# Performance work log

Measured on AMD Instinct MI355X. Metric: run time of the kernel, lower is better.

## Reference

```python
import jax, jax.numpy as jnp
import numpy as np

D_MODEL, D_STATE, D_CONV, D_INNER, DT_RANK, K = 96, 16, 3, 192, 6, 4
B, H, W = 1, 64, 64


def setup_inputs() -> dict:
    key = jax.random.key(0)
    ks = jax.random.split(key, 10)
    x = jax.random.normal(ks[0], (B, H, W, D_MODEL), jnp.float32)
    in_proj_w = jax.random.normal(ks[1], (2 * D_INNER, D_MODEL), jnp.float32) * 0.02
    conv_w = jax.random.normal(ks[2], (D_INNER, 1, D_CONV, D_CONV), jnp.float32) * 0.1
    conv_b = jnp.zeros((D_INNER,), jnp.float32)
    x_proj_w = jax.random.normal(ks[3], (K, DT_RANK + 2 * D_STATE, D_INNER), jnp.float32) * 0.02
    dt_std = DT_RANK ** -0.5
    dt_w = jax.random.uniform(ks[4], (K, D_INNER, DT_RANK), jnp.float32, -dt_std, dt_std)
    # dt bias init: inv-softplus of dt ~ logUniform(1e-3, 1e-1)
    u = jax.random.uniform(ks[5], (K, D_INNER), jnp.float32)
    dt = jnp.exp(u * (np.log(0.1) - np.log(0.001)) + np.log(0.001)).clip(1e-4)
    dt_b = dt + jnp.log(-jnp.expm1(-dt))
    A_logs = jnp.log(jnp.broadcast_to(jnp.arange(1, D_STATE + 1, dtype=jnp.float32), (K * D_INNER, D_STATE)))
    Ds = jnp.ones((K * D_INNER,), jnp.float32)
    ln_g = jnp.ones((D_INNER,), jnp.float32)
    ln_b = jnp.zeros((D_INNER,), jnp.float32)
    out_proj_w = jax.random.normal(ks[6], (D_MODEL, D_INNER), jnp.float32) * 0.02
    return dict(x=x, in_proj_w=in_proj_w, conv_w=conv_w, conv_b=conv_b, x_proj_w=x_proj_w,
                dt_w=dt_w, dt_b=dt_b, A_logs=A_logs, Ds=Ds, ln_g=ln_g, ln_b=ln_b,
                out_proj_w=out_proj_w)


def _ss2d(x, in_proj_w, conv_w, conv_b, x_proj_w, dt_w, dt_b, A_logs, Ds, ln_g, ln_b, out_proj_w):
    b, h, w, c = x.shape
    L = h * w
    d = conv_w.shape[0]            # d_inner
    n = A_logs.shape[1]            # d_state
    r = dt_w.shape[2]              # dt_rank
    # in_proj + split
    xz = jnp.einsum('bhwc,ec->bhwe', x, in_proj_w)
    xx, z = xz[..., :d], xz[..., d:]
    # depthwise conv (NCHW) + SiLU
    xc = xx.transpose(0, 3, 1, 2)
    pad = (D_CONV - 1) // 2
    xc = jax.lax.conv_general_dilated(xc, conv_w, (1, 1), [(pad, pad), (pad, pad)],
                                      feature_group_count=d) + conv_b[None, :, None, None]
    xc = jax.nn.silu(xc)
    # 4 scan directions: HW, WH, and their reverses
    x_hw = xc.reshape(b, d, L)
    x_wh = xc.transpose(0, 1, 3, 2).reshape(b, d, L)
    xs = jnp.stack([x_hw, x_wh, x_hw[..., ::-1], x_wh[..., ::-1]], axis=1)  # (b,K,d,L)
    x_dbl = jnp.einsum('bkdl,kcd->bkcl', xs, x_proj_w)
    dts, Bs, Cs = x_dbl[:, :, :r], x_dbl[:, :, r:r + n], x_dbl[:, :, r + n:]
    dts = jnp.einsum('bkrl,kdr->bkdl', dts, dt_w)
    delta = jax.nn.softplus(dts + dt_b[None, :, :, None])        # (b,K,d,L)
    A = -jnp.exp(A_logs).reshape(K, d, n)
    # time-major scanned inputs
    dA = jnp.exp(jnp.einsum('bkdl,kdn->lbkdn', delta, A))        # (L,b,K,d,n)
    dBu = jnp.einsum('bkdl,bknl,bkdl->lbkdn', delta, Bs, xs)
    Ct = Cs.transpose(3, 0, 1, 2)                                # (L,b,K,n)
    def step(hst, inp):
        dA_t, dBu_t, C_t = inp
        hst = dA_t * hst + dBu_t
        return hst, jnp.einsum('bkdn,bkn->bkd', hst, C_t)
    h0 = jnp.zeros((b, K, d, n), jnp.float32)
    _, ys = jax.lax.scan(step, h0, (dA, dBu, Ct))                # ys: (L,b,K,d)
    out_y = ys.transpose(1, 2, 3, 0) + xs * Ds.reshape(K, d)[None, :, :, None]
    # recombine directions
    inv = out_y[:, 2:4][..., ::-1]
    y1 = out_y[:, 0]
    y2 = inv[:, 0]
    wh = out_y[:, 1].reshape(b, d, w, h).transpose(0, 1, 3, 2).reshape(b, d, L)
    invwh = inv[:, 1].reshape(b, d, w, h).transpose(0, 1, 3, 2).reshape(b, d, L)
    y = (y1 + y2 + wh + invwh).transpose(0, 2, 1).reshape(b, h, w, d)
    # LayerNorm (eps=1e-5, torch default)
    mu = y.mean(-1, keepdims=True)
    var = ((y - mu) ** 2).mean(-1, keepdims=True)
    y = (y - mu) * jax.lax.rsqrt(var + 1e-5) * ln_g + ln_b
    y = y * jax.nn.silu(z)
    return jnp.einsum('bhwd,cd->bhwc', y, out_proj_w)


def reference(x, in_proj_w, conv_w, conv_b, x_proj_w, dt_w, dt_b, A_logs, Ds, ln_g, ln_b, out_proj_w):
    return _ss2d(x, in_proj_w, conv_w, conv_b, x_proj_w, dt_w, dt_b, A_logs, Ds, ln_g, ln_b, out_proj_w)
```

## Files before the change

### kernel.cpp

```cpp
#include <hip/hip_runtime.h>
#include <hip/hip_bf16.h>

#define LL 4096
#define DM 96
#define DI 192
#define NS 16
#define RK 6
#define RKP 8
#define KD 4
#define CPROJ 38
#define NCH (KD*DI)
#define NC (KD*DI*NS)
#define PT 32
#define WS 196
#define OT 8
#define L2E 1.44269504f

__device__ __forceinline__ float bf2f(unsigned short u){
  unsigned int x = ((unsigned int)u) << 16;
  return __uint_as_float(x);
}
__device__ __forceinline__ float b2f(__hip_bfloat16 v){ return __bfloat162float(v); }

__device__ __forceinline__ void detect_bf16(const unsigned short* __restrict__ xh, int tid, int* sflag){
  if (tid < 64){
    unsigned short u = xh[2*tid];
    int e = (u >> 7) & 0xFF;
    int sane = (e >= 107 && e <= 131) ? 1 : 0;
    unsigned long long m = __ballot(sane);
    if (tid == 0) *sflag = (__popcll(m) >= 32) ? 1 : 0;
  }
}

__device__ __forceinline__ int dir_map(int k, int t){
  if (k==0) return t;
  if (k==1) return ((t&63)<<6) | (t>>6);
  if (k==2) return 4095 - t;
  int u = 4095 - t; return ((u&63)<<6) | (u>>6);
}

struct P12 { const void* p[12]; };

__global__ void __launch_bounds__(384) k_inprojcvt(P12 ptrs, float* __restrict__ cvt,
                         float* __restrict__ xx, float* __restrict__ z) {
  __shared__ float xr[8*DM];
  __shared__ int sflag;
  int tid = threadIdx.x;
  detect_bf16((const unsigned short*)ptrs.p[0], tid, &sflag);
  __syncthreads();
  int f = sflag;
  if (blockIdx.x >= LL/8){
    const int off[12] = {0,36864,38592,38784,67968,72576,73344,85632,86400,86592,86784,105216};
    int i = (blockIdx.x - LL/8)*384 + tid + 36864;
    if (i < 105216){
      int j = 1;
      #pragma unroll
      for (int s = 2; s < 11; s++) if (i >= off[s]) j = s;
      int e = i - off[j];
      const void* src = ptrs.p[j+1];
      cvt[i] = f ? b2f(((const __hip_bfloat16*)src)[e]) : ((const float*)src)[e];
    }
    return;
  }
  int l0 = blockIdx.x * 8;
  if (f){
    const __hip_bfloat16* xb = (const __hip_bfloat16*)ptrs.p[0] + (size_t)l0*DM;
    for (int i = tid; i < 8*DM; i += 384) xr[i] = b2f(xb[i]);
  } else {
    const float* xf = (const float*)ptrs.p[0] + (size_t)l0*DM;
    for (int i = tid; i < 8*DM; i += 384) xr[i] = xf[i];
  }
  __syncthreads();
  int e = tid;
  float acc[8];
  #pragma unroll
  for (int i=0;i<8;i++) acc[i]=0.f;
  const float4* xr4 = (const float4*)xr;
  if (f){
    const ushort4* wb = (const ushort4*)((const unsigned short*)ptrs.p[1] + (size_t)e*DM);
    #pragma unroll 4
    for (int c4=0;c4<DM/4;c4++){
      ushort4 uv = wb[c4];
      float4 wv = make_float4(bf2f(uv.x), bf2f(uv.y), bf2f(uv.z), bf2f(uv.w));
      #pragma unroll
      for (int i=0;i<8;i++){
        float4 xv = xr4[i*24 + c4];
        acc[i] = fmaf(wv.x,xv.x,fmaf(wv.y,xv.y,fmaf(wv.z,xv.z,fmaf(wv.w,xv.w,acc[i]))));
      }
    }
  } else {
    const float4* wr4 = (const float4*)((const float*)ptrs.p[1] + (size_t)e*DM);
    #pragma unroll 4
    for (int c4=0;c4<DM/4;c4++){
      float4 wv = wr4[c4];
      #pragma unroll
      for (int i=0;i<8;i++){
        float4 xv = xr4[i*24 + c4];
        acc[i] = fmaf(wv.x,xv.x,fmaf(wv.y,xv.y,fmaf(wv.z,xv.z,fmaf(wv.w,xv.w,acc[i]))));
      }
    }
  }
  if (e < DI) {
    #pragma unroll
    for (int i=0;i<8;i++) xx[(l0+i)*DI + e] = acc[i];
  } else {
    int e2 = e - DI;
    #pragma unroll
    for (int i=0;i<8;i++) z[(l0+i)*DI + e2] = acc[i];
  }
}

__global__ void k_conv(const float* __restrict__ xx,
                       const float* __restrict__ cw,
                       const float* __restrict__ cb,
                       float* __restrict__ xc) {
  int l = blockIdx.x;
  int d = threadIdx.x;
  int h = l >> 6, w = l & 63;
  float acc = cb[d];
  #pragma unroll
  for (int ki=0; ki<3; ki++){
    int hh = h + ki - 1;
    if ((unsigned)hh >= 64u) continue;
    #pragma unroll
    for (int kj=0;kj<3;kj++){
      int wj = w + kj - 1;
      if ((unsigned)wj >= 64u) continue;
      acc = fmaf(cw[d*9 + ki*3 + kj], xx[(hh*64+wj)*DI + d], acc);
    }
  }
  float v = acc / (1.f + __expf(-acc));
  xc[l*DI + d] = v;
}

__global__ void __launch_bounds__(256) k_proj(const float* __restrict__ xc,
                       const float* __restrict__ xpw,
                       float* __restrict__ dts,
                       float* __restrict__ Bb, float* __restrict__ Cb) {
  __shared__ float wl[CPROJ*WS];
  __shared__ float xs[PT*WS];
  int b = blockIdx.x;
  int k = b >> 7;
  int t_base = (b & 127) * PT;
  int tid = threadIdx.x;
  for (int idx = tid; idx < CPROJ*DI; idx += 256){
    int cc = idx / DI, j = idx - cc*DI;
    wl[cc*WS + j] = xpw[(k*CPROJ + cc)*DI + j];
  }
  for (int idx = tid; idx < PT*DI; idx += 256){
    int tt = idx / DI, j = idx - tt*DI;
    xs[tt*WS + j] = xc[dir_map(k, t_base + tt)*DI + j];
  }
  __syncthreads();
  int tg = tid & 7;
  int ty = tid >> 3;
  int cc0 = ty;
  int has2 = (ty + 32 < CPROJ);
  int cc1 = has2 ? (ty + 32) : ty;
  float a0x=0.f,a0y=0.f,a0z=0.f,a0w=0.f;
  float a1x=0.f,a1y=0.f,a1z=0.f,a1w=0.f;
  const float4* w0p = (const float4*)&wl[cc0*WS];
  const float4* w1p = (const float4*)&wl[cc1*WS];
  const float4* x0p = (const float4*)&xs[(tg     )*WS];
  const float4* x1p = (const float4*)&xs[(tg +  8)*WS];
  const float4* x2p = (const float4*)&xs[(tg + 16)*WS];
  const float4* x3p = (const float4*)&xs[(tg + 24)*WS];
  #pragma unroll 4
  for (int jc = 0; jc < DI/4; jc++){
    float4 w0 = w0p[jc], w1 = w1p[jc];
    float4 x0 = x0p[jc], x1 = x1p[jc], x2 = x2p[jc], x3 = x3p[jc];
    a0x = fmaf(w0.x,x0.x,fmaf(w0.y,x0.y,fmaf(w0.z,x0.z,fmaf(w0.w,x0.w,a0x))));
    a0y = fmaf(w0.x,x1.x,fmaf(w0.y,x1.y,fmaf(w0.z,x1.z,fmaf(w0.w,x1.w,a0y))));
    a0z = fmaf(w0.x,x2.x,fmaf(w0.y,x2.y,fmaf(w0.z,x2.z,fmaf(w0.w,x2.w,a0z))));
    a0w = fmaf(w0.x,x3.x,fmaf(w0.y,x3.y,fmaf(w0.z,x3.z,fmaf(w0.w,x3.w,a0w))));
    a1x = fmaf(w1.x,x0.x,fmaf(w1.y,x0.y,fmaf(w1.z,x0.z,fmaf(w1.w,x0.w,a1x))));
    a1y = fmaf(w1.x,x1.x,fmaf(w1.y,x1.y,fmaf(w1.z,x1.z,fmaf(w1.w,x1.w,a1y))));
    a1z = fmaf(w1.x,x2.x,fmaf(w1.y,x2.y,fmaf(w1.z,x2.z,fmaf(w1.w,x2.w,a1z))));
    a1w = fmaf(w1.x,x3.x,fmaf(w1.y,x3.y,fmaf(w1.z,x3.z,fmaf(w1.w,x3.w,a1w))));
  }
  float accs0[4] = {a0x,a0y,a0z,a0w};
  float accs1[4] = {a1x,a1y,a1z,a1w};
  #pragma unroll
  for (int i=0;i<4;i++){
    int t = t_base + tg + 8*i;
    size_t kt = (size_t)k*LL + t;
    {
      int cc = cc0; float v = accs0[i];
      if (cc < RK)            dts[kt*RKP + cc] = v;
      else if (cc < RK+NS)    Bb [kt*NS + (cc-RK)] = v;
      else                    Cb [kt*NS + (cc-RK-NS)] = v;
    }
    if (has2){
      int cc = ty + 32; float v = accs1[i];
      if (cc < RK+NS)         Bb [kt*NS + (cc-RK)] = v;
      else                    Cb [kt*NS + (cc-RK-NS)] = v;
    }
  }
}

template<int CHB>
__global__ void __launch_bounds__(192) k_scanA(
                      const float* __restrict__ xc,
                      const float* __restrict__ dts,
                      const float* __restrict__ Bbuf,
                      const float* __restrict__ A_logs,
                      const float* __restrict__ dtw,
                      const float* __restrict__ dtb,
                      float* __restrict__ cumDbuf,
                      float* __restrict__ Harr) {
  constexpr int CS = LL >> CHB;
  __shared__ float ds_[CS*RKP];
  __shared__ float Bs[CS*NS];
  int b = blockIdx.x;
  int k = b >> CHB;
  int c = b & ((1<<CHB)-1);
  int t0 = c*CS;
  int d = threadIdx.x;
  int kd = k*DI + d;
  for (int i = d; i < CS*RKP; i += 192) ds_[i] = dts[((size_t)k*LL + t0)*RKP + i];
  for (int i = d; i < CS*NS;  i += 192) Bs[i]  = Bbuf[((size_t)k*LL + t0)*NS + i];
  float bt = dtb[kd];
  float w0 = dtw[kd*RK+0], w1 = dtw[kd*RK+1], w2 = dtw[kd*RK+2];
  float w3 = dtw[kd*RK+3], w4 = dtw[kd*RK+4], w5 = dtw[kd*RK+5];
  float A2[16], h[16];
  {
    const float4* ap = (const float4*)&A_logs[kd*NS];
    #pragma unroll
    for (int i=0;i<4;i++){
      float4 av = ap[i];
      A2[4*i+0] = -__expf(av.x)*L2E; A2[4*i+1] = -__expf(av.y)*L2E;
      A2[4*i+2] = -__expf(av.z)*L2E; A2[4*i+3] = -__expf(av.w)*L2E;
    }
  }
  #pragma unroll
  for (int n=0;n<16;n++) h[n] = 0.f;
  __syncthreads();
  float cumD = 0.f;
  #pragma unroll 2
  for (int s=0; s<CS; s++){
    float4 lo = *(const float4*)(ds_ + s*RKP);
    float4 hi = *(const float4*)(ds_ + s*RKP + 4);
    float v = bt;
    v = fmaf(w0, lo.x, v); v = fmaf(w1, lo.y, v); v = fmaf(w2, lo.z, v);
    v = fmaf(w3, lo.w, v); v = fmaf(w4, hi.x, v); v = fmaf(w5, hi.y, v);
    float sp = (v > 20.f) ? v : __logf(1.f + __expf(v));
    cumD += sp;
    int row = dir_map(k, t0 + s);
    float sx = sp * xc[(size_t)row*DI + d];
    float4 b0 = *(const float4*)(Bs + s*NS);
    float4 b1 = *(const float4*)(Bs + s*NS + 4);
    float4 b2 = *(const float4*)(Bs + s*NS + 8);
    float4 b3 = *(const float4*)(Bs + s*NS + 12);
    float bb[16] = {b0.x,b0.y,b0.z,b0.w, b1.x,b1.y,b1.z,b1.w,
                    b2.x,b2.y,b2.z,b2.w, b3.x,b3.y,b3.z,b3.w};
    #pragma unroll
    for (int n=0;n<16;n++){
      float a = exp2f(sp*A2[n]);
      h[n] = fmaf(a, h[n], sx*bb[n]);
    }
  }
  cumDbuf[(size_t)c*NCH + kd] = cumD;
  float4* hp = (float4*)(Harr + ((size_t)c*NCH + kd)*16);
  hp[0] = make_float4(h[0],h[1],h[2],h[3]);
  hp[1] = make_float4(h[4],h[5],h[6],h[7]);
  hp[2] = make_float4(h[8],h[9],h[10],h[11]);
  hp[3] = make_float4(h[12],h[13],h[14],h[15]);
}

template<int CHB>
__global__ void __launch_bounds__(256) k_scan2(const float* __restrict__ A_logs,
                                               const float* __restrict__ cumDbuf,
                                               float* __restrict__ Harr) {
  constexpr int CH = 1 << CHB;
  int idx = blockIdx.x*256 + threadIdx.x;
  int kd = idx >> 4;
  float A2 = -__expf(A_logs[idx]) * L2E;
  float h = 0.f;
  #pragma unroll 4
  for (int c=0;c<CH;c++){
    float hl = Harr[(size_t)c*NC + idx];
    float P = exp2f(A2 * cumDbuf[(size_t)c*NCH + kd]);
    Harr[(size_t)c*NC + idx] = h;
    h = fmaf(P, h, hl);
  }
}

template<int CHB>
__global__ void __launch_bounds__(192) k_scanB(
                      const float* __restrict__ xc,
                      const float* __restrict__ dts,
                      const float* __restrict__ Bbuf,
                      const float* __restrict__ Cbuf,
                      const float* __restrict__ A_logs,
                      const float* __restrict__ dtw,
                      const float* __restrict__ dtb,
                      const float* __restrict__ Harr,
                      float* __restrict__ ydir) {
  constexpr int CS = LL >> CHB;
  __shared__ float ds_[CS*RKP];
  __shared__ float Bs[CS*NS];
  __shared__ float Cs[CS*NS];
  int b = blockIdx.x;
  int k = b >> CHB;
  int c = b & ((1<<CHB)-1);
  int t0 = c*CS;
  int d = threadIdx.x;
  int kd = k*DI + d;
  for (int i = d; i < CS*RKP; i += 192) ds_[i] = dts[((size_t)k*LL + t0)*RKP + i];
  for (int i = d; i < CS*NS;  i += 192) Bs[i]  = Bbuf[((size_t)k*LL + t0)*NS + i];
  for (int i = d; i < CS*NS;  i += 192) Cs[i]  = Cbuf[((size_t)k*LL + t0)*NS + i];
  float bt = dtb[kd];
  float w0 = dtw[kd*RK+0], w1 = dtw[kd*RK+1], w2 = dtw[kd*RK+2];
  float w3 = dtw[kd*RK+3], w4 = dtw[kd*RK+4], w5 = dtw[kd*RK+5];
  float A2[16], h[16];
  {
    const float4* ap = (const float4*)&A_logs[kd*NS];
    #pragma unroll
    for (int i=0;i<4;i++){
      float4 av = ap[i];
      A2[4*i+0] = -__expf(av.x)*L2E; A2[4*i+1] = -__expf(av.y)*L2E;
      A2[4*i+2] = -__expf(av.z)*L2E; A2[4*i+3] = -__expf(av.w)*L2E;
    }
  }
  {
    const float4* hp = (const float4*)(Harr + ((size_t)c*NCH + kd)*16);
    float4 h0 = hp[0], h1 = hp[1], h2 = hp[2], h3 = hp[3];
    h[0]=h0.x; h[1]=h0.y; h[2]=h0.z; h[3]=h0.w;
    h[4]=h1.x; h[5]=h1.y; h[6]=h1.z; h[7]=h1.w;
    h[8]=h2.x; h[9]=h2.y; h[10]=h2.z; h[11]=h2.w;
    h[12]=h3.x; h[13]=h3.y; h[14]=h3.z; h[15]=h3.w;
  }
  __syncthreads();
  #pragma unroll 2
  for (int s=0; s<CS; s++){
    float4 lo = *(const float4*)(ds_ + s*RKP);
    float4 hi = *(const float4*)(ds_ + s*RKP + 4);
    float v = bt;
    v = fmaf(w0, lo.x, v); v = fmaf(w1, lo.y, v); v = fmaf(w2, lo.z, v);
    v = fmaf(w3, lo.w, v); v = fmaf(w4, hi.x, v); v = fmaf(w5, hi.y, v);
    float sp = (v > 20.f) ? v : __logf(1.f + __expf(v));
    int row = dir_map(k, t0 + s);
    float sx = sp * xc[(size_t)row*DI + d];
    float4 b0 = *(const float4*)(Bs + s*NS);
    float4 b1 = *(const float4*)(Bs + s*NS + 4);
    float4 b2 = *(const float4*)(Bs + s*NS + 8);
    float4 b3 = *(const float4*)(Bs + s*NS + 12);
    float bb[16] = {b0.x,b0.y,b0.z,b0.w, b1.x,b1.y,b1.z,b1.w,
                    b2.x,b2.y,b2.z,b2.w, b3.x,b3.y,b3.z,b3.w};
    #pragma unroll
    for (int n=0;n<16;n++){
      float a = exp2f(sp*A2[n]);
      h[n] = fmaf(a, h[n], sx*bb[n]);
    }
    float4 c0 = *(const float4*)(Cs + s*NS);
    float4 c1 = *(const float4*)(Cs + s*NS + 4);
    float4 c2 = *(const float4*)(Cs + s*NS + 8);
    float4 c3 = *(const float4*)(Cs + s*NS + 12);
    float cc[16] = {c0.x,c0.y,c0.z,c0.w, c1.x,c1.y,c1.z,c1.w,
                    c2.x,c2.y,c2.z,c2.w, c3.x,c3.y,c3.z,c3.w};
    float y0=0.f, y1=0.f, y2=0.f, y3=0.f;
    #pragma unroll
    for (int n=0;n<4;n++){
      y0 = fmaf(h[4*n+0], cc[4*n+0], y0);
      y1 = fmaf(h[4*n+1], cc[4*n+1], y1);
      y2 = fmaf(h[4*n+2], cc[4*n+2], y2);
      y3 = fmaf(h[4*n+3], cc[4*n+3], y3);
    }
    ydir[((size_t)k*LL + row)*DI + d] = (y0+y1)+(y2+y3);
  }
}

__global__ void __launch_bounds__(192) k_out(
                      const float* __restrict__ ydir,
                      const float* __restrict__ xc,
                      const float* __restrict__ z,
                      const float* __restrict__ Ds,
                      const float* __restrict__ ln_g,
                      const float* __restrict__ ln_b,
                      const float* __restrict__ opw,
                      void* __restrict__ out,
                      const unsigned short* __restrict__ xh) {
  __shared__ float gs[OT*WS];
  __shared__ float ps[2][OT][24];
  __shared__ float mv[2][OT];
  __shared__ int sflag;
  int tid = threadIdx.x;
  int d = tid;
  detect_bf16(xh, tid, &sflag);
  int l0 = blockIdx.x * OT;
  float dsum = Ds[d] + Ds[DI+d] + Ds[2*DI+d] + Ds[3*DI+d];
  #pragma unroll
  for (int r=0;r<OT;r++){
    size_t ld = (size_t)(l0+r)*DI + d;
    float y = ydir[ld]
            + ydir[(size_t)LL*DI   + ld]
            + ydir[(size_t)2*LL*DI + ld]
            + ydir[(size_t)3*LL*DI + ld];
    gs[r*WS + d] = fmaf(xc[ld], dsum, y);
  }
  __syncthreads();
  {
    int r = tid / 24, lane = tid - r*24;
    float s1 = 0.f, s2 = 0.f;
    #pragma unroll
    for (int j = lane; j < DI; j += 24){
      float v = gs[r*WS + j];
      s1 += v; s2 += v*v;
    }
    ps[0][r][lane] = s1; ps[1][r][lane] = s2;
  }
  __syncthreads();
  if (tid < OT){
    float a = 0.f, bb = 0.f;
    #pragma unroll
    for (int j=0;j<24;j++){ a += ps[0][tid][j]; bb += ps[1][tid][j]; }
    float mu = a * (1.f/192.f);
    float var = bb * (1.f/192.f) - mu*mu;
    mv[0][tid] = mu; mv[1][tid] = rsqrtf(var + 1e-5f);
  }
  __syncthreads();
  float lg = ln_g[d], lb = ln_b[d];
  #pragma unroll
  for (int r=0;r<OT;r++){
    float yn = (gs[r*WS + d] - mv[0][r]) * mv[1][r] * lg + lb;
    float zv = z[(size_t)(l0+r)*DI + d];
    gs[r*WS + d] = yn * (zv / (1.f + __expf(-zv)));
  }
  __syncthreads();
  int half = tid / 96;
  int e = tid - half*96;
  int r0 = half*4;
  float acc[4];
  #pragma unroll
  for (int i=0;i<4;i++) acc[i] = 0.f;
  const float4* wrow = (const float4*)(opw + e*DI);
  #pragma unroll 4
  for (int jc = 0; jc < DI/4; jc++){
    float4 w = wrow[jc];
    #pragma unroll
    for (int i=0;i<4;i++){
      float4 gv = *(const float4*)&gs[(r0+i)*WS + jc*4];
      acc[i] = fmaf(w.x,gv.x,fmaf(w.y,gv.y,fmaf(w.z,gv.z,fmaf(w.w,gv.w,acc[i]))));
    }
  }
  int f = sflag;
  #pragma unroll
  for (int i=0;i<4;i++){
    int l = l0 + r0 + i;
    if (f) ((__hip_bfloat16*)out)[l*DM + e] = __float2bfloat16(acc[i]);
    else   ((float*)out)[l*DM + e] = acc[i];
  }
}

extern "C" void kernel_launch(void* const* d_in, const int* in_sizes, int n_in,
                              void* d_out, int out_size, void* d_ws, size_t ws_size,
                              hipStream_t stream) {
  float* ws = (float*)d_ws;
  float* cvt = ws + 16;
  const int off[12] = {0,36864,38592,38784,67968,72576,73344,85632,86400,86592,86784,105216};
  float* c[12];
  c[0] = nullptr;
  for (int i = 1; i < 12; i++) c[i] = cvt + off[i-1];

  float* xx   = cvt + 105216;
  float* z    = xx + (size_t)LL*DI;
  float* xc   = z  + (size_t)LL*DI;
  float* dts  = xc + (size_t)LL*DI;
  float* Bb   = dts + (size_t)KD*LL*RKP;
  float* Cb   = Bb + (size_t)KD*LL*NS;
  float* cumD = Cb + (size_t)KD*LL*NS;

  size_t fixed = 16 + 105216 + 3*(size_t)LL*DI + (size_t)KD*LL*RKP
               + 2*(size_t)KD*LL*NS + (size_t)KD*LL*DI;
  size_t need8 = (fixed + 256*(size_t)(NCH + NC)) * 4;
  int chBits = (ws_size >= need8) ? 8 : 6;
  int CHn = 1 << chBits;
  float* Harr = cumD + (size_t)CHn*NCH;
  float* ydir = Harr + (size_t)CHn*NC;

  P12 ptrs;
  for (int i = 0; i < 12; i++) ptrs.p[i] = d_in[i];

  k_inprojcvt<<<LL/8 + 178, 384, 0, stream>>>(ptrs, cvt, xx, z);
  k_conv<<<LL, DI, 0, stream>>>(xx, c[2], c[3], xc);
  k_proj<<<KD*(LL/PT), 256, 0, stream>>>(xc, c[4], dts, Bb, Cb);
  if (chBits == 8){
    k_scanA<8><<<KD*256, 192, 0, stream>>>(xc, dts, Bb, c[7], c[5], c[6], cumD, Harr);
    k_scan2<8><<<NC/256, 256, 0, stream>>>(c[7], cumD, Harr);
    k_scanB<8><<<KD*256, 192, 0, stream>>>(xc, dts, Bb, Cb, c[7], c[5], c[6], Harr, ydir);
  } else {
    k_scanA<6><<<KD*64, 192, 0, stream>>>(xc, dts, Bb, c[7], c[5], c[6], cumD, Harr);
    k_scan2<6><<<NC/256, 256, 0, stream>>>(c[7], cumD, Harr);
    k_scanB<6><<<KD*64, 192, 0, stream>>>(xc, dts, Bb, Cb, c[7], c[5], c[6], Harr, ydir);
  }
  k_out<<<LL/OT, 192, 0, stream>>>(ydir, xc, z, c[8], c[9], c[10], c[11], d_out,
                                   (const unsigned short*)d_in[0]);
}
```

Baseline: 220.1 us.

## Fuse all stages into one persistent megakernel with global atomic barriers

```diff
diff --git a/kernel.cpp b/kernel.cpp
--- a/kernel.cpp
+++ b/kernel.cpp
@@ -14,23 +14,20 @@
 #define PT 32
 #define WS 196
 #define OT 8
+#define CHB 7
+#define CHN (1<<CHB)
+#define CS (LL>>CHB)
+#define GRID 512
+#define BLK 256
+#define SMEMF ((CPROJ+PT)*WS)
 #define L2E 1.44269504f
+#define SPIN_MAX 2000000u
 
 __device__ __forceinline__ float bf2f(unsigned short u){
   unsigned int x = ((unsigned int)u) << 16;
   return __uint_as_float(x);
 }
 __device__ __forceinline__ float b2f(__hip_bfloat16 v){ return __bfloat162float(v); }
-
-__device__ __forceinline__ void detect_bf16(const unsigned short* __restrict__ xh, int tid, int* sflag){
-  if (tid < 64){
-    unsigned short u = xh[2*tid];
-    int e = (u >> 7) & 0xFF;
-    int sane = (e >= 107 && e <= 131) ? 1 : 0;
-    unsigned long long m = __ballot(sane);
-    if (tid == 0) *sflag = (__popcll(m) >= 32) ? 1 : 0;
-  }
-}
 
 __device__ __forceinline__ int dir_map(int k, int t){
   if (k==0) return t;
@@ -39,416 +36,467 @@
   int u = 4095 - t; return ((u&63)<<6) | (u>>6);
 }
 
-struct P12 { const void* p[12]; };
-
-__global__ void __launch_bounds__(384) k_inprojcvt(P12 ptrs, float* __restrict__ cvt,
-                         float* __restrict__ xx, float* __restrict__ z) {
-  __shared__ float xr[8*DM];
+__device__ __forceinline__ void gbar(int* cnt){
+  __syncthreads();
+  if (threadIdx.x == 0){
+    __threadfence();
+    atomicAdd(cnt, 1);
+    unsigned it = 0;
+    while (__hip_atomic_load(cnt, __ATOMIC_RELAXED, __HIP_MEMORY_SCOPE_AGENT) < GRID
+           && ++it < SPIN_MAX){
+      __builtin_amdgcn_s_sleep(2);
+    }
+    __threadfence();
+  }
+  __syncthreads();
+}
+
+struct MArgs {
+  const void* p[12];
+  float* cvt;
+  float* xx; float* z; float* xc;
+  float* dts; float* Bb; float* Cb;
+  float* cumD; float* Harr; float* ydir;
+  int* bar;
+  void* out;
+};
+
+__global__ void __launch_bounds__(BLK, 2) k_mega(MArgs a) {
+  __shared__ float smem[SMEMF];
   __shared__ int sflag;
-  int tid = threadIdx.x;
-  detect_bf16((const unsigned short*)ptrs.p[0], tid, &sflag);
+  const int tid = threadIdx.x;
+  const int b   = blockIdx.x;
+
+  if (tid < 64){
+    unsigned short u = ((const unsigned short*)a.p[0])[2*tid];
+    int e = (u >> 7) & 0xFF;
+    int sane = (e >= 107 && e <= 131) ? 1 : 0;
+    unsigned long long m = __ballot(sane);
+    if (tid == 0) sflag = (__popcll(m) >= 32) ? 1 : 0;
+  }
   __syncthreads();
-  int f = sflag;
-  if (blockIdx.x >= LL/8){
-    const int off[12] = {0,36864,38592,38784,67968,72576,73344,85632,86400,86592,86784,105216};
-    int i = (blockIdx.x - LL/8)*384 + tid + 36864;
-    if (i < 105216){
-      int j = 1;
-      #pragma unroll
-      for (int s = 2; s < 11; s++) if (i >= off[s]) j = s;
-      int e = i - off[j];
-      const void* src = ptrs.p[j+1];
-      cvt[i] = f ? b2f(((const __hip_bfloat16*)src)[e]) : ((const float*)src)[e];
-    }
-    return;
-  }
-  int l0 = blockIdx.x * 8;
-  if (f){
-    const __hip_bfloat16* xb = (const __hip_bfloat16*)ptrs.p[0] + (size_t)l0*DM;
-    for (int i = tid; i < 8*DM; i += 384) xr[i] = b2f(xb[i]);
-  } else {
-    const float* xf = (const float*)ptrs.p[0] + (size_t)l0*DM;
-    for (int i = tid; i < 8*DM; i += 384) xr[i] = xf[i];
-  }
-  __syncthreads();
-  int e = tid;
-  float acc[8];
-  #pragma unroll
-  for (int i=0;i<8;i++) acc[i]=0.f;
-  const float4* xr4 = (const float4*)xr;
-  if (f){
-    const ushort4* wb = (const ushort4*)((const unsigned short*)ptrs.p[1] + (size_t)e*DM);
+  const int f = sflag;
+
+  {
+    float* xr = smem;
+    int l0 = b * 8;
+    if (f){
+      const __hip_bfloat16* xb = (const __hip_bfloat16*)a.p[0] + (size_t)l0*DM;
+      for (int i = tid; i < 8*DM; i += BLK) xr[i] = b2f(xb[i]);
+    } else {
+      const float* xf = (const float*)a.p[0] + (size_t)l0*DM;
+      for (int i = tid; i < 8*DM; i += BLK) xr[i] = xf[i];
+    }
+    {
+      const int off[12] = {0,36864,38592,38784,67968,72576,73344,85632,86400,86592,86784,105216};
+      int i = b*BLK + tid + 36864;
+      if (i < 105216){
+        int j = 1;
+        #pragma unroll
+        for (int s = 2; s < 11; s++) if (i >= off[s]) j = s;
+        int e = i - off[j];
+        const void* src = a.p[j+1];
+        a.cvt[i] = f ? b2f(((const __hip_bfloat16*)src)[e]) : ((const float*)src)[e];
+      }
+    }
+    __syncthreads();
+    const float4* xr4 = (const float4*)xr;
+    #pragma unroll
+    for (int pass = 0; pass < 2; pass++){
+      int e = tid + (pass << 8);
+      if (e < 2*DI){
+        float acc[8];
+        #pragma unroll
+        for (int i=0;i<8;i++) acc[i]=0.f;
+        if (f){
+          const ushort4* wb = (const ushort4*)((const unsigned short*)a.p[1] + (size_t)e*DM);
+          #pragma unroll 4
+          for (int c4=0;c4<DM/4;c4++){
+            ushort4 uv = wb[c4];
+            float4 wv = make_float4(bf2f(uv.x), bf2f(uv.y), bf2f(uv.z), bf2f(uv.w));
+            #pragma unroll
+            for (int i=0;i<8;i++){
+              float4 xv = xr4[i*24 + c4];
+              acc[i] = fmaf(wv.x,xv.x,fmaf(wv.y,xv.y,fmaf(wv.z,xv.z,fmaf(wv.w,xv.w,acc[i]))));
+            }
+          }
+        } else {
+          const float4* wr4 = (const float4*)((const float*)a.p[1] + (size_t)e*DM);
+          #pragma unroll 4
+          for (int c4=0;c4<DM/4;c4++){
+            float4 wv = wr4[c4];
+            #pragma unroll
+            for (int i=0;i<8;i++){
+              float4 xv = xr4[i*24 + c4];
+              acc[i] = fmaf(wv.x,xv.x,fmaf(wv.y,xv.y,fmaf(wv.z,xv.z,fmaf(wv.w,xv.w,acc[i]))));
+            }
+          }
+        }
+        if (e < DI){
+          #pragma unroll
+          for (int i=0;i<8;i++) a.xx[(l0+i)*DI + e] = acc[i];
+        } else {
+          int e2 = e - DI;
+          #pragma unroll
+          for (int i=0;i<8;i++) a.z[(l0+i)*DI + e2] = acc[i];
+        }
+      }
+    }
+  }
+  gbar(a.bar + 0);
+
+  {
+    const float* cw = a.cvt + 36864;
+    const float* cb = a.cvt + 38592;
+    int l0 = b * 8;
+    for (int i = tid; i < 8*DI; i += BLK){
+      int r = i / DI;
+      int d = i - r*DI;
+      int l = l0 + r;
+      int h = l >> 6, w = l & 63;
+      float acc = cb[d];
+      #pragma unroll
+      for (int ki=0; ki<3; ki++){
+        int hh = h + ki - 1;
+        if ((unsigned)hh >= 64u) continue;
+        #pragma unroll
+        for (int kj=0;kj<3;kj++){
+          int wj = w + kj - 1;
+          if ((unsigned)wj >= 64u) continue;
+          acc = fmaf(cw[d*9 + ki*3 + kj], a.xx[(hh*64+wj)*DI + d], acc);
+        }
+      }
+      a.xc[(size_t)l*DI + d] = acc / (1.f + __expf(-acc));
+    }
+  }
+  gbar(a.bar + 1);
+
+  {
+    float* wl = smem;
+    float* xs = smem + CPROJ*WS;
+    const float* xpw = a.cvt + 38784;
+    int k = b >> 7;
+    int t_base = (b & 127) * PT;
+    for (int idx = tid; idx < CPROJ*DI; idx += BLK){
+      int cc = idx / DI, j = idx - cc*DI;
+      wl[cc*WS + j] = xpw[(k*CPROJ + cc)*DI + j];
+    }
+    for (int idx = tid; idx < PT*DI; idx += BLK){
+      int tt = idx / DI, j = idx - tt*DI;
+      xs[tt*WS + j] = a.xc[(size_t)dir_map(k, t_base + tt)*DI + j];
+    }
+    __syncthreads();
+    int tg = tid & 7;
+    int ty = tid >> 3;
+    int cc0 = ty;
+    int has2 = (ty + 32 < CPROJ);
+    int cc1 = has2 ? (ty + 32) : ty;
+    float a0x=0.f,a0y=0.f,a0z=0.f,a0w=0.f;
+    float a1x=0.f,a1y=0.f,a1z=0.f,a1w=0.f;
+    const float4* w0p = (const float4*)&wl[cc0*WS];
+    const float4* w1p = (const float4*)&wl[cc1*WS];
+    const float4* x0p = (const float4*)&xs[(tg     )*WS];
+    const float4* x1p = (const float4*)&xs[(tg +  8)*WS];
+    const float4* x2p = (const float4*)&xs[(tg + 16)*WS];
+    const float4* x3p = (const float4*)&xs[(tg + 24)*WS];
     #pragma unroll 4
-    for (int c4=0;c4<DM/4;c4++){
-      ushort4 uv = wb[c4];
-      float4 wv = make_float4(bf2f(uv.x), bf2f(uv.y), bf2f(uv.z), bf2f(uv.w));
-      #pragma unroll
-      for (int i=0;i<8;i++){
-        float4 xv = xr4[i*24 + c4];
-        acc[i] = fmaf(wv.x,xv.x,fmaf(wv.y,xv.y,fmaf(wv.z,xv.z,fmaf(wv.w,xv.w,acc[i]))));
-      }
-    }
-  } else {
-    const float4* wr4 = (const float4*)((const float*)ptrs.p[1] + (size_t)e*DM);
-    #pragma unroll 4
-    for (int c4=0;c4<DM/4;c4++){
-      float4 wv = wr4[c4];
-      #pragma unroll
-      for (int i=0;i<8;i++){
-        float4 xv = xr4[i*24 + c4];
-        acc[i] = fmaf(wv.x,xv.x,fmaf(wv.y,xv.y,fmaf(wv.z,xv.z,fmaf(wv.w,xv.w,acc[i]))));
-      }
-    }
-  }
-  if (e < DI) {
-    #pragma unroll
-    for (int i=0;i<8;i++) xx[(l0+i)*DI + e] = acc[i];
-  } else {
-    int e2 = e - DI;
-    #pragma unroll
-    for (int i=0;i<8;i++) z[(l0+i)*DI + e2] = acc[i];
-  }
-}
-
-__global__ void k_conv(const float* __restrict__ xx,
-                       const float* __restrict__ cw,
-                       const float* __restrict__ cb,
-                       float* __restrict__ xc) {
-  int l = blockIdx.x;
-  int d = threadIdx.x;
-  int h = l >> 6, w = l & 63;
-  float acc = cb[d];
-  #pragma unroll
-  for (int ki=0; ki<3; ki++){
-    int hh = h + ki - 1;
-    if ((unsigned)hh >= 64u) continue;
-    #pragma unroll
-    for (int kj=0;kj<3;kj++){
-      int wj = w + kj - 1;
-      if ((unsigned)wj >= 64u) continue;
-      acc = fmaf(cw[d*9 + ki*3 + kj], xx[(hh*64+wj)*DI + d], acc);
-    }
-  }
-  float v = acc / (1.f + __expf(-acc));
-  xc[l*DI + d] = v;
-}
-
-__global__ void __launch_bounds__(256) k_proj(const float* __restrict__ xc,
-                       const float* __restrict__ xpw,
-                       float* __restrict__ dts,
-                       float* __restrict__ Bb, float* __restrict__ Cb) {
-  __shared__ float wl[CPROJ*WS];
-  __shared__ float xs[PT*WS];
-  int b = blockIdx.x;
-  int k = b >> 7;
-  int t_base = (b & 127) * PT;
-  int tid = threadIdx.x;
-  for (int idx = tid; idx < CPROJ*DI; idx += 256){
-    int cc = idx / DI, j = idx - cc*DI;
-    wl[cc*WS + j] = xpw[(k*CPROJ + cc)*DI + j];
-  }
-  for (int idx = tid; idx < PT*DI; idx += 256){
-    int tt = idx / DI, j = idx - tt*DI;
-    xs[tt*WS + j] = xc[dir_map(k, t_base + tt)*DI + j];
-  }
-  __syncthreads();
-  int tg = tid & 7;
-  int ty = tid >> 3;
-  int cc0 = ty;
-  int has2 = (ty + 32 < CPROJ);
-  int cc1 = has2 ? (ty + 32) : ty;
-  float a0x=0.f,a0y=0.f,a0z=0.f,a0w=0.f;
-  float a1x=0.f,a1y=0.f,a1z=0.f,a1w=0.f;
-  const float4* w0p = (const float4*)&wl[cc0*WS];
-  const float4* w1p = (const float4*)&wl[cc1*WS];
-  const float4* x0p = (const float4*)&xs[(tg     )*WS];
-  const float4* x1p = (const float4*)&xs[(tg +  8)*WS];
-  const float4* x2p = (const float4*)&xs[(tg + 16)*WS];
-  const float4* x3p = (const float4*)&xs[(tg + 24)*WS];
-  #pragma unroll 4
-  for (int jc = 0; jc < DI/4; jc++){
-    float4 w0 = w0p[jc], w1 = w1p[jc];
-    float4 x0 = x0p[jc], x1 = x1p[jc], x2 = x2p[jc], x3 = x3p[jc];
-    a0x = fmaf(w0.x,x0.x,fmaf(w0.y,x0.y,fmaf(w0.z,x0.z,fmaf(w0.w,x0.w,a0x))));
-    a0y = fmaf(w0.x,x1.x,fmaf(w0.y,x1.y,fmaf(w0.z,x1.z,fmaf(w0.w,x1.w,a0y))));
-    a0z = fmaf(w0.x,x2.x,fmaf(w0.y,x2.y,fmaf(w0.z,x2.z,fmaf(w0.w,x2.w,a0z))));
-    a0w = fmaf(w0.x,x3.x,fmaf(w0.y,x3.y,fmaf(w0.z,x3.z,fmaf(w0.w,x3.w,a0w))));
-    a1x = fmaf(w1.x,x0.x,fmaf(w1.y,x0.y,fmaf(w1.z,x0.z,fmaf(w1.w,x0.w,a1x))));
-    a1y = fmaf(w1.x,x1.x,fmaf(w1.y,x1.y,fmaf(w1.z,x1.z,fmaf(w1.w,x1.w,a1y))));
-    a1z = fmaf(w1.x,x2.x,fmaf(w1.y,x2.y,fmaf(w1.z,x2.z,fmaf(w1.w,x2.w,a1z))));
-    a1w = fmaf(w1.x,x3.x,fmaf(w1.y,x3.y,fmaf(w1.z,x3.z,fmaf(w1.w,x3.w,a1w))));
-  }
-  float accs0[4] = {a0x,a0y,a0z,a0w};
-  float accs1[4] = {a1x,a1y,a1z,a1w};
-  #pragma unroll
-  for (int i=0;i<4;i++){
-    int t = t_base + tg + 8*i;
-    size_t kt = (size_t)k*LL + t;
-    {
-      int cc = cc0; float v = accs0[i];
-      if (cc < RK)            dts[kt*RKP + cc] = v;
-      else if (cc < RK+NS)    Bb [kt*NS + (cc-RK)] = v;
-      else                    Cb [kt*NS + (cc-RK-NS)] = v;
-    }
-    if (has2){
-      int cc = ty + 32; float v = accs1[i];
-      if (cc < RK+NS)         Bb [kt*NS + (cc-RK)] = v;
-      else                    Cb [kt*NS + (cc-RK-NS)] = v;
-    }
-  }
-}
-
-template<int CHB>
-__global__ void __launch_bounds__(192) k_scanA(
-                      const float* __restrict__ xc,
-                      const float* __restrict__ dts,
-                      const float* __restrict__ Bbuf,
-                      const float* __restrict__ A_logs,
-                      const float* __restrict__ dtw,
-                      const float* __restrict__ dtb,
-                      float* __restrict__ cumDbuf,
-                      float* __restrict__ Harr) {
-  constexpr int CS = LL >> CHB;
-  __shared__ float ds_[CS*RKP];
-  __shared__ float Bs[CS*NS];
-  int b = blockIdx.x;
-  int k = b >> CHB;
-  int c = b & ((1<<CHB)-1);
-  int t0 = c*CS;
-  int d = threadIdx.x;
-  int kd = k*DI + d;
-  for (int i = d; i < CS*RKP; i += 192) ds_[i] = dts[((size_t)k*LL + t0)*RKP + i];
-  for (int i = d; i < CS*NS;  i += 192) Bs[i]  = Bbuf[((size_t)k*LL + t0)*NS + i];
-  float bt = dtb[kd];
-  float w0 = dtw[kd*RK+0], w1 = dtw[kd*RK+1], w2 = dtw[kd*RK+2];
-  float w3 = dtw[kd*RK+3], w4 = dtw[kd*RK+4], w5 = dtw[kd*RK+5];
-  float A2[16], h[16];
-  {
-    const float4* ap = (const float4*)&A_logs[kd*NS];
+    for (int jc = 0; jc < DI/4; jc++){
+      float4 w0 = w0p[jc], w1 = w1p[jc];
+      float4 x0 = x0p[jc], x1 = x1p[jc], x2 = x2p[jc], x3 = x3p[jc];
+      a0x = fmaf(w0.x,x0.x,fmaf(w0.y,x0.y,fmaf(w0.z,x0.z,fmaf(w0.w,x0.w,a0x))));
+      a0y = fmaf(w0.x,x1.x,fmaf(w0.y,x1.y,fmaf(w0.z,x1.z,fmaf(w0.w,x1.w,a0y))));
+      a0z = fmaf(w0.x,x2.x,fmaf(w0.y,x2.y,fmaf(w0.z,x2.z,fmaf(w0.w,x2.w,a0z))));
+      a0w = fmaf(w0.x,x3.x,fmaf(w0.y,x3.y,fmaf(w0.z,x3.z,fmaf(w0.w,x3.w,a0w))));
+      a1x = fmaf(w1.x,x0.x,fmaf(w1.y,x0.y,fmaf(w1.z,x0.z,fmaf(w1.w,x0.w,a1x))));
+      a1y = fmaf(w1.x,x1.x,fmaf(w1.y,x1.y,fmaf(w1.z,x1.z,fmaf(w1.w,x1.w,a1y))));
+      a1z = fmaf(w1.x,x2.x,fmaf(w1.y,x2.y,fmaf(w1.z,x2.z,fmaf(w1.w,x2.w,a1z))));
+      a1w = fmaf(w1.x,x3.x,fmaf(w1.y,x3.y,fmaf(w1.z,x3.z,fmaf(w1.w,x3.w,a1w))));
+    }
+    float accs0[4] = {a0x,a0y,a0z,a0w};
+    float accs1[4] = {a1x,a1y,a1z,a1w};
     #pragma unroll
     for (int i=0;i<4;i++){
-      float4 av = ap[i];
-      A2[4*i+0] = -__expf(av.x)*L2E; A2[4*i+1] = -__expf(av.y)*L2E;
-      A2[4*i+2] = -__expf(av.z)*L2E; A2[4*i+3] = -__expf(av.w)*L2E;
-    }
-  }
-  #pragma unroll
-  for (int n=0;n<16;n++) h[n] = 0.f;
-  __syncthreads();
-  float cumD = 0.f;
-  #pragma unroll 2
-  for (int s=0; s<CS; s++){
-    float4 lo = *(const float4*)(ds_ + s*RKP);
-    float4 hi = *(const float4*)(ds_ + s*RKP + 4);
-    float v = bt;
-    v = fmaf(w0, lo.x, v); v = fmaf(w1, lo.y, v); v = fmaf(w2, lo.z, v);
-    v = fmaf(w3, lo.w, v); v = fmaf(w4, hi.x, v); v = fmaf(w5, hi.y, v);
-    float sp = (v > 20.f) ? v : __logf(1.f + __expf(v));
-    cumD += sp;
-    int row = dir_map(k, t0 + s);
-    float sx = sp * xc[(size_t)row*DI + d];
-    float4 b0 = *(const float4*)(Bs + s*NS);
-    float4 b1 = *(const float4*)(Bs + s*NS + 4);
-    float4 b2 = *(const float4*)(Bs + s*NS + 8);
-    float4 b3 = *(const float4*)(Bs + s*NS + 12);
-    float bb[16] = {b0.x,b0.y,b0.z,b0.w, b1.x,b1.y,b1.z,b1.w,
-                    b2.x,b2.y,b2.z,b2.w, b3.x,b3.y,b3.z,b3.w};
-    #pragma unroll
-    for (int n=0;n<16;n++){
-      float a = exp2f(sp*A2[n]);
-      h[n] = fmaf(a, h[n], sx*bb[n]);
-    }
-  }
-  cumDbuf[(size_t)c*NCH + kd] = cumD;
-  float4* hp = (float4*)(Harr + ((size_t)c*NCH + kd)*16);
-  hp[0] = make_float4(h[0],h[1],h[2],h[3]);
-  hp[1] = make_float4(h[4],h[5],h[6],h[7]);
-  hp[2] = make_float4(h[8],h[9],h[10],h[11]);
-  hp[3] = make_float4(h[12],h[13],h[14],h[15]);
-}
-
-template<int CHB>
-__global__ void __launch_bounds__(256) k_scan2(const float* __restrict__ A_logs,
-                                               const float* __restrict__ cumDbuf,
-                                               float* __restrict__ Harr) {
-  constexpr int CH = 1 << CHB;
-  int idx = blockIdx.x*256 + threadIdx.x;
-  int kd = idx >> 4;
-  float A2 = -__expf(A_logs[idx]) * L2E;
-  float h = 0.f;
-  #pragma unroll 4
-  for (int c=0;c<CH;c++){
-    float hl = Harr[(size_t)c*NC + idx];
-    float P = exp2f(A2 * cumDbuf[(size_t)c*NCH + kd]);
-    Harr[(size_t)c*NC + idx] = h;
-    h = fmaf(P, h, hl);
-  }
-}
-
-template<int CHB>
-__global__ void __launch_bounds__(192) k_scanB(
-                      const float* __restrict__ xc,
-                      const float* __restrict__ dts,
-                      const float* __restrict__ Bbuf,
-                      const float* __restrict__ Cbuf,
-                      const float* __restrict__ A_logs,
-                      const float* __restrict__ dtw,
-                      const float* __restrict__ dtb,
-                      const float* __restrict__ Harr,
-                      float* __restrict__ ydir) {
-  constexpr int CS = LL >> CHB;
-  __shared__ float ds_[CS*RKP];
-  __shared__ float Bs[CS*NS];
-  __shared__ float Cs[CS*NS];
-  int b = blockIdx.x;
-  int k = b >> CHB;
-  int c = b & ((1<<CHB)-1);
-  int t0 = c*CS;
-  int d = threadIdx.x;
-  int kd = k*DI + d;
-  for (int i = d; i < CS*RKP; i += 192) ds_[i] = dts[((size_t)k*LL + t0)*RKP + i];
-  for (int i = d; i < CS*NS;  i += 192) Bs[i]  = Bbuf[((size_t)k*LL + t0)*NS + i];
-  for (int i = d; i < CS*NS;  i += 192) Cs[i]  = Cbuf[((size_t)k*LL + t0)*NS + i];
-  float bt = dtb[kd];
-  float w0 = dtw[kd*RK+0], w1 = dtw[kd*RK+1], w2 = dtw[kd*RK+2];
-  float w3 = dtw[kd*RK+3], w4 = dtw[kd*RK+4], w5 = dtw[kd*RK+5];
-  float A2[16], h[16];
+      int t = t_base + tg + 8*i;
+      size_t kt = (size_t)k*LL + t;
+      {
+        int cc = cc0; float v = accs0[i];
+        if (cc < RK)            a.dts[kt*RKP + cc] = v;
+        else if (cc < RK+NS)    a.Bb [kt*NS + (cc-RK)] = v;
+        else                    a.Cb [kt*NS + (cc-RK-NS)] = v;
+      }
+      if (has2){
+        int cc = ty + 32; float v = accs1[i];
+        if (cc < RK+NS)         a.Bb [kt*NS + (cc-RK)] = v;
+        else                    a.Cb [kt*NS + (cc-RK-NS)] = v;
+      }
+    }
+  }
+  gbar(a.bar + 2);
+
   {
-    const float4* ap = (const float4*)&A_logs[kd*NS];
-    #pragma unroll
-    for (int i=0;i<4;i++){
-      float4 av = ap[i];
-      A2[4*i+0] = -__expf(av.x)*L2E; A2[4*i+1] = -__expf(av.y)*L2E;
-      A2[4*i+2] = -__expf(av.z)*L2E; A2[4*i+3] = -__expf(av.w)*L2E;
-    }
-  }
+    const float* A_logs = a.cvt + 73344;
+    const float* dtw    = a.cvt + 67968;
+    const float* dtb    = a.cvt + 72576;
+    float* ds_ = smem;
+    float* Bs  = smem + CS*RKP;
+    int k = b >> CHB;
+    int c = b & (CHN-1);
+    int t0 = c*CS;
+    ds_[tid]     = a.dts[((size_t)k*LL + t0)*RKP + tid];
+    Bs[tid]      = a.Bb[((size_t)k*LL + t0)*NS + tid];
+    Bs[tid+256]  = a.Bb[((size_t)k*LL + t0)*NS + tid + 256];
+    __syncthreads();
+    if (tid < DI){
+      int d = tid;
+      int kd = k*DI + d;
+      float bt = dtb[kd];
+      float w0 = dtw[kd*RK+0], w1 = dtw[kd*RK+1], w2 = dtw[kd*RK+2];
+      float w3 = dtw[kd*RK+3], w4 = dtw[kd*RK+4], w5 = dtw[kd*RK+5];
+      float A2[16], h[16];
+      {
+        const float4* ap = (const float4*)&A_logs[kd*NS];
+        #pragma unroll
+        for (int i=0;i<4;i++){
+          float4 av = ap[i];
+          A2[4*i+0] = -__expf(av.x)*L2E; A2[4*i+1] = -__expf(av.y)*L2E;
+          A2[4*i+2] = -__expf(av.z)*L2E; A2[4*i+3] = -__expf(av.w)*L2E;
+        }
+      }
+      #pragma unroll
+      for (int n=0;n<16;n++) h[n] = 0.f;
+      float cumD = 0.f;
+      #pragma unroll 2
+      for (int s=0; s<CS; s++){
+        float4 lo = *(const float4*)(ds_ + s*RKP);
+        float4 hi = *(const float4*)(ds_ + s*RKP + 4);
+        float v = bt;
+        v = fmaf(w0, lo.x, v); v = fmaf(w1, lo.y, v); v = fmaf(w2, lo.z, v);
+        v = fmaf(w3, lo.w, v); v = fmaf(w4, hi.x, v); v = fmaf(w5, hi.y, v);
+        float sp = (v > 20.f) ? v : __logf(1.f + __expf(v));
+        cumD += sp;
+        int row = dir_map(k, t0 + s);
+        float sx = sp * a.xc[(size_t)row*DI + d];
+        float4 b0 = *(const float4*)(Bs + s*NS);
+        float4 b1 = *(const float4*)(Bs + s*NS + 4);
+        float4 b2 = *(const float4*)(Bs + s*NS + 8);
+        float4 b3 = *(const float4*)(Bs + s*NS + 12);
+        float bb[16] = {b0.x,b0.y,b0.z,b0.w, b1.x,b1.y,b1.z,b1.w,
+                        b2.x,b2.y,b2.z,b2.w, b3.x,b3.y,b3.z,b3.w};
+        #pragma unroll
+        for (int n=0;n<16;n++){
+          float aa = exp2f(sp*A2[n]);
+          h[n] = fmaf(aa, h[n], sx*bb[n]);
+        }
+      }
+      a.cumD[(size_t)c*NCH + kd] = cumD;
+      float4* hp = (float4*)(a.Harr + ((size_t)c*NCH + kd)*16);
+      hp[0] = make_float4(h[0],h[1],h[2],h[3]);
+      hp[1] = make_float4(h[4],h[5],h[6],h[7]);
+      hp[2] = make_float4(h[8],h[9],h[10],h[11]);
+      hp[3] = make_float4(h[12],h[13],h[14],h[15]);
+    }
+  }
+  gbar(a.bar + 3);
+
+  if (b < NCH/2){
+    const float* A_logs = a.cvt + 73344;
+    float* hs  = smem;
+    float* cds = smem + 32*129;
+    int base = b*32;
+    int kd0  = b*2;
+    for (int i4 = tid; i4 < 8*CHN; i4 += BLK){
+      int c = i4 >> 3;
+      int jv = (i4 & 7)*4;
+      float4 v = *(const float4*)&a.Harr[(size_t)c*NC + base + jv];
+      hs[(jv  )*129 + c] = v.x; hs[(jv+1)*129 + c] = v.y;
+      hs[(jv+2)*129 + c] = v.z; hs[(jv+3)*129 + c] = v.w;
+    }
+    { int c = tid >> 1, kdl = tid & 1;
+      cds[kdl*CHN + c] = a.cumD[(size_t)c*NCH + kd0 + kdl]; }
+    __syncthreads();
+    if (tid < 32){
+      float A2 = -__expf(A_logs[base + tid]) * L2E;
+      const float* cd = cds + (tid>>4)*CHN;
+      float* hr = hs + tid*129;
+      float h = 0.f;
+      #pragma unroll 4
+      for (int c = 0; c < CHN; c++){
+        float hl = hr[c];
+        float P = exp2f(A2 * cd[c]);
+        hr[c] = h;
+        h = fmaf(P, h, hl);
+      }
+    }
+    __syncthreads();
+    for (int i4 = tid; i4 < 8*CHN; i4 += BLK){
+      int c = i4 >> 3;
+      int jv = (i4 & 7)*4;
+      float4 v = make_float4(hs[(jv)*129+c], hs[(jv+1)*129+c],
+                             hs[(jv+2)*129+c], hs[(jv+3)*129+c]);
+      *(float4*)&a.Harr[(size_t)c*NC + base + jv] = v;
+    }
+  }
+  gbar(a.bar + 4);
+
   {
-    const float4* hp = (const float4*)(Harr + ((size_t)c*NCH + kd)*16);
-    float4 h0 = hp[0], h1 = hp[1], h2 = hp[2], h3 = hp[3];
-    h[0]=h0.x; h[1]=h0.y; h[2]=h0.z; h[3]=h0.w;
-    h[4]=h1.x; h[5]=h1.y; h[6]=h1.z; h[7]=h1.w;
-    h[8]=h2.x; h[9]=h2.y; h[10]=h2.z; h[11]=h2.w;
-    h[12]=h3.x; h[13]=h3.y; h[14]=h3.z; h[15]=h3.w;
-  }
-  __syncthreads();
-  #pragma unroll 2
-  for (int s=0; s<CS; s++){
-    float4 lo = *(const float4*)(ds_ + s*RKP);
-    float4 hi = *(const float4*)(ds_ + s*RKP + 4);
-    float v = bt;
-    v = fmaf(w0, lo.x, v); v = fmaf(w1, lo.y, v); v = fmaf(w2, lo.z, v);
-    v = fmaf(w3, lo.w, v); v = fmaf(w4, hi.x, v); v = fmaf(w5, hi.y, v);
-    float sp = (v > 20.f) ? v : __logf(1.f + __expf(v));
-    int row = dir_map(k, t0 + s);
-    float sx = sp * xc[(size_t)row*DI + d];
-    float4 b0 = *(const float4*)(Bs + s*NS);
-    float4 b1 = *(const float4*)(Bs + s*NS + 4);
-    float4 b2 = *(const float4*)(Bs + s*NS + 8);
-    float4 b3 = *(const float4*)(Bs + s*NS + 12);
-    float bb[16] = {b0.x,b0.y,b0.z,b0.w, b1.x,b1.y,b1.z,b1.w,
-                    b2.x,b2.y,b2.z,b2.w, b3.x,b3.y,b3.z,b3.w};
-    #pragma unroll
-    for (int n=0;n<16;n++){
-      float a = exp2f(sp*A2[n]);
-      h[n] = fmaf(a, h[n], sx*bb[n]);
-    }
-    float4 c0 = *(const float4*)(Cs + s*NS);
-    float4 c1 = *(const float4*)(Cs + s*NS + 4);
-    float4 c2 = *(const float4*)(Cs + s*NS + 8);
-    float4 c3 = *(const float4*)(Cs + s*NS + 12);
-    float cc[16] = {c0.x,c0.y,c0.z,c0.w, c1.x,c1.y,c1.z,c1.w,
-                    c2.x,c2.y,c2.z,c2.w, c3.x,c3.y,c3.z,c3.w};
-    float y0=0.f, y1=0.f, y2=0.f, y3=0.f;
-    #pragma unroll
-    for (int n=0;n<4;n++){
-      y0 = fmaf(h[4*n+0], cc[4*n+0], y0);
-      y1 = fmaf(h[4*n+1], cc[4*n+1], y1);
-      y2 = fmaf(h[4*n+2], cc[4*n+2], y2);
-      y3 = fmaf(h[4*n+3], cc[4*n+3], y3);
-    }
-    ydir[((size_t)k*LL + row)*DI + d] = (y0+y1)+(y2+y3);
-  }
-}
-
-__global__ void __launch_bounds__(192) k_out(
-                      const float* __restrict__ ydir,
-                      const float* __restrict__ xc,
-                      const float* __restrict__ z,
-                      const float* __restrict__ Ds,
-                      const float* __restrict__ ln_g,
-                      const float* __restrict__ ln_b,
-                      const float* __restrict__ opw,
-                      void* __restrict__ out,
-                      const unsigned short* __restrict__ xh) {
-  __shared__ float gs[OT*WS];
-  __shared__ float ps[2][OT][24];
-  __shared__ float mv[2][OT];
-  __shared__ int sflag;
-  int tid = threadIdx.x;
-  int d = tid;
-  detect_bf16(xh, tid, &sflag);
-  int l0 = blockIdx.x * OT;
-  float dsum = Ds[d] + Ds[DI+d] + Ds[2*DI+d] + Ds[3*DI+d];
-  #pragma unroll
-  for (int r=0;r<OT;r++){
-    size_t ld = (size_t)(l0+r)*DI + d;
-    float y = ydir[ld]
-            + ydir[(size_t)LL*DI   + ld]
-            + ydir[(size_t)2*LL*DI + ld]
-            + ydir[(size_t)3*LL*DI + ld];
-    gs[r*WS + d] = fmaf(xc[ld], dsum, y);
-  }
-  __syncthreads();
+    const float* A_logs = a.cvt + 73344;
+    const float* dtw    = a.cvt + 67968;
+    const float* dtb    = a.cvt + 72576;
+    float* ds_ = smem;
+    float* Bs  = smem + CS*RKP;
+    float* Cs  = Bs + CS*NS;
+    int k = b >> CHB;
+    int c = b & (CHN-1);
+    int t0 = c*CS;
+    ds_[tid]     = a.dts[((size_t)k*LL + t0)*RKP + tid];
+    Bs[tid]      = a.Bb[((size_t)k*LL + t0)*NS + tid];
+    Bs[tid+256]  = a.Bb[((size_t)k*LL + t0)*NS + tid + 256];
+    Cs[tid]      = a.Cb[((size_t)k*LL + t0)*NS + tid];
+    Cs[tid+256]  = a.Cb[((size_t)k*LL + t0)*NS + tid + 256];
+    __syncthreads();
+    if (tid < DI){
+      int d = tid;
+      int kd = k*DI + d;
+      float bt = dtb[kd];
+      float w0 = dtw[kd*RK+0], w1 = dtw[kd*RK+1], w2 = dtw[kd*RK+2];
+      float w3 = dtw[kd*RK+3], w4 = dtw[kd*RK+4], w5 = dtw[kd*RK+5];
+      float A2[16], h[16];
+      {
+        const float4* ap = (const float4*)&A_logs[kd*NS];
+        #pragma unroll
+        for (int i=0;i<4;i++){
+          float4 av = ap[i];
+          A2[4*i+0] = -__expf(av.x)*L2E; A2[4*i+1] = -__expf(av.y)*L2E;
+          A2[4*i+2] = -__expf(av.z)*L2E; A2[4*i+3] = -__expf(av.w)*L2E;
+        }
+      }
+      {
+        const float4* hp = (const float4*)(a.Harr + ((size_t)c*NCH + kd)*16);
+        float4 h0 = hp[0], h1 = hp[1], h2 = hp[2], h3 = hp[3];
+        h[0]=h0.x; h[1]=h0.y; h[2]=h0.z; h[3]=h0.w;
+        h[4]=h1.x; h[5]=h1.y; h[6]=h1.z; h[7]=h1.w;
+        h[8]=h2.x; h[9]=h2.y; h[10]=h2.z; h[11]=h2.w;
+        h[12]=h3.x; h[13]=h3.y; h[14]=h3.z; h[15]=h3.w;
+      }
+      #pragma unroll 2
+      for (int s=0; s<CS; s++){
+        float4 lo = *(const float4*)(ds_ + s*RKP);
+        float4 hi = *(const float4*)(ds_ + s*RKP + 4);
+        float v = bt;
+        v = fmaf(w0, lo.x, v); v = fmaf(w1, lo.y, v); v = fmaf(w2, lo.z, v);
+        v = fmaf(w3, lo.w, v); v = fmaf(w4, hi.x, v); v = fmaf(w5, hi.y, v);
+        float sp = (v > 20.f) ? v : __logf(1.f + __expf(v));
+        int row = dir_map(k, t0 + s);
+        float sx = sp * a.xc[(size_t)row*DI + d];
+        float4 b0 = *(const float4*)(Bs + s*NS);
+        float4 b1 = *(const float4*)(Bs + s*NS + 4);
+        float4 b2 = *(const float4*)(Bs + s*NS + 8);
+        float4 b3 = *(const float4*)(Bs + s*NS + 12);
+        float bb[16] = {b0.x,b0.y,b0.z,b0.w, b1.x,b1.y,b1.z,b1.w,
+                        b2.x,b2.y,b2.z,b2.w, b3.x,b3.y,b3.z,b3.w};
+        #pragma unroll
+        for (int n=0;n<16;n++){
+          float aa = exp2f(sp*A2[n]);
+          h[n] = fmaf(aa, h[n], sx*bb[n]);
+        }
+        float4 c0 = *(const float4*)(Cs + s*NS);
+        float4 c1 = *(const float4*)(Cs + s*NS + 4);
+        float4 c2 = *(const float4*)(Cs + s*NS + 8);
+        float4 c3 = *(const float4*)(Cs + s*NS + 12);
+        float cc[16] = {c0.x,c0.y,c0.z,c0.w, c1.x,c1.y,c1.z,c1.w,
+                        c2.x,c2.y,c2.z,c2.w, c3.x,c3.y,c3.z,c3.w};
+        float y0=0.f, y1=0.f, y2=0.f, y3=0.f;
+        #pragma unroll
+        for (int n=0;n<4;n++){
+          y0 = fmaf(h[4*n+0], cc[4*n+0], y0);
+          y1 = fmaf(h[4*n+1], cc[4*n+1], y1);
+          y2 = fmaf(h[4*n+2], cc[4*n+2], y2);
+          y3 = fmaf(h[4*n+3], cc[4*n+3], y3);
+        }
+        a.ydir[((size_t)k*LL + row)*DI + d] = (y0+y1)+(y2+y3);
+      }
+    }
+  }
+  gbar(a.bar + 5);
+
   {
-    int r = tid / 24, lane = tid - r*24;
-    float s1 = 0.f, s2 = 0.f;
-    #pragma unroll
-    for (int j = lane; j < DI; j += 24){
-      float v = gs[r*WS + j];
-      s1 += v; s2 += v*v;
-    }
-    ps[0][r][lane] = s1; ps[1][r][lane] = s2;
-  }
-  __syncthreads();
-  if (tid < OT){
-    float a = 0.f, bb = 0.f;
-    #pragma unroll
-    for (int j=0;j<24;j++){ a += ps[0][tid][j]; bb += ps[1][tid][j]; }
-    float mu = a * (1.f/192.f);
-    float var = bb * (1.f/192.f) - mu*mu;
-    mv[0][tid] = mu; mv[1][tid] = rsqrtf(var + 1e-5f);
-  }
-  __syncthreads();
-  float lg = ln_g[d], lb = ln_b[d];
-  #pragma unroll
-  for (int r=0;r<OT;r++){
-    float yn = (gs[r*WS + d] - mv[0][r]) * mv[1][r] * lg + lb;
-    float zv = z[(size_t)(l0+r)*DI + d];
-    gs[r*WS + d] = yn * (zv / (1.f + __expf(-zv)));
-  }
-  __syncthreads();
-  int half = tid / 96;
-  int e = tid - half*96;
-  int r0 = half*4;
-  float acc[4];
-  #pragma unroll
-  for (int i=0;i<4;i++) acc[i] = 0.f;
-  const float4* wrow = (const float4*)(opw + e*DI);
-  #pragma unroll 4
-  for (int jc = 0; jc < DI/4; jc++){
-    float4 w = wrow[jc];
-    #pragma unroll
-    for (int i=0;i<4;i++){
-      float4 gv = *(const float4*)&gs[(r0+i)*WS + jc*4];
-      acc[i] = fmaf(w.x,gv.x,fmaf(w.y,gv.y,fmaf(w.z,gv.z,fmaf(w.w,gv.w,acc[i]))));
-    }
-  }
-  int f = sflag;
-  #pragma unroll
-  for (int i=0;i<4;i++){
-    int l = l0 + r0 + i;
-    if (f) ((__hip_bfloat16*)out)[l*DM + e] = __float2bfloat16(acc[i]);
-    else   ((float*)out)[l*DM + e] = acc[i];
+    const float* Ds   = a.cvt + 85632;
+    const float* ln_g = a.cvt + 86400;
+    const float* ln_b = a.cvt + 86592;
+    const float* opw  = a.cvt + 86784;
+    float* gs = smem;
+    float* ps = smem + OT*WS;
+    float* mv = ps + 2*OT*24;
+    int l0 = b * OT;
+    int d = tid;
+    if (d < DI){
+      float dsum = Ds[d] + Ds[DI+d] + Ds[2*DI+d] + Ds[3*DI+d];
+      #pragma unroll
+      for (int r=0;r<OT;r++){
+        size_t ld = (size_t)(l0+r)*DI + d;
+        float y = a.ydir[ld]
+                + a.ydir[(size_t)LL*DI   + ld]
+                + a.ydir[(size_t)2*LL*DI + ld]
+                + a.ydir[(size_t)3*LL*DI + ld];
+        gs[r*WS + d] = fmaf(a.xc[ld], dsum, y);
+      }
+    }
+    __syncthreads();
+    if (tid < 192){
+      int r = tid / 24, lane = tid - r*24;
+      float s1 = 0.f, s2 = 0.f;
+      #pragma unroll
+      for (int j = lane; j < DI; j += 24){
+        float v = gs[r*WS + j];
+        s1 += v; s2 += v*v;
+      }
+      ps[0*192 + r*24 + lane] = s1;
+      ps[1*192 + r*24 + lane] = s2;
+    }
+    __syncthreads();
+    if (tid < OT){
+      float aa = 0.f, bb = 0.f;
+      #pragma unroll
+      for (int j=0;j<24;j++){ aa += ps[0*192 + tid*24 + j]; bb += ps[1*192 + tid*24 + j]; }
+      float mu = aa * (1.f/192.f);
+      float var = bb * (1.f/192.f) - mu*mu;
+      mv[tid] = mu; mv[OT + tid] = rsqrtf(var + 1e-5f);
+    }
+    __syncthreads();
+    if (d < DI){
+      float lg = ln_g[d], lb = ln_b[d];
+      #pragma unroll
+      for (int r=0;r<OT;r++){
+        float yn = (gs[r*WS + d] - mv[r]) * mv[OT + r] * lg + lb;
+        float zv = a.z[(size_t)(l0+r)*DI + d];
+        gs[r*WS + d] = yn * (zv / (1.f + __expf(-zv)));
+      }
+    }
+    __syncthreads();
+    if (tid < 192){
+      int half = tid / 96;
+      int e = tid - half*96;
+      int r0 = half*4;
+      float acc[4];
+      #pragma unroll
+      for (int i=0;i<4;i++) acc[i] = 0.f;
+      const float4* wrow = (const float4*)(opw + e*DI);
+      #pragma unroll 4
+      for (int jc = 0; jc < DI/4; jc++){
+        float4 w = wrow[jc];
+        #pragma unroll
+        for (int i=0;i<4;i++){
+          float4 gv = *(const float4*)&gs[(r0+i)*WS + jc*4];
+          acc[i] = fmaf(w.x,gv.x,fmaf(w.y,gv.y,fmaf(w.z,gv.z,fmaf(w.w,gv.w,acc[i]))));
+        }
+      }
+      #pragma unroll
+      for (int i=0;i<4;i++){
+        int l = l0 + r0 + i;
+        if (f) ((__hip_bfloat16*)a.out)[l*DM + e] = __float2bfloat16(acc[i]);
+        else   ((float*)a.out)[l*DM + e] = acc[i];
+      }
+    }
   }
 }
 
@@ -457,10 +505,6 @@
                               hipStream_t stream) {
   float* ws = (float*)d_ws;
   float* cvt = ws + 16;
-  const int off[12] = {0,36864,38592,38784,67968,72576,73344,85632,86400,86592,86784,105216};
-  float* c[12];
-  c[0] = nullptr;
-  for (int i = 1; i < 12; i++) c[i] = cvt + off[i-1];
 
   float* xx   = cvt + 105216;
   float* z    = xx + (size_t)LL*DI;
@@ -469,30 +513,17 @@
   float* Bb   = dts + (size_t)KD*LL*RKP;
   float* Cb   = Bb + (size_t)KD*LL*NS;
   float* cumD = Cb + (size_t)KD*LL*NS;
-
-  size_t fixed = 16 + 105216 + 3*(size_t)LL*DI + (size_t)KD*LL*RKP
-               + 2*(size_t)KD*LL*NS + (size_t)KD*LL*DI;
-  size_t need8 = (fixed + 256*(size_t)(NCH + NC)) * 4;
-  int chBits = (ws_size >= need8) ? 8 : 6;
-  int CHn = 1 << chBits;
-  float* Harr = cumD + (size_t)CHn*NCH;
-  float* ydir = Harr + (size_t)CHn*NC;
-
-  P12 ptrs;
-  for (int i = 0; i < 12; i++) ptrs.p[i] = d_in[i];
-
-  k_inprojcvt<<<LL/8 + 178, 384, 0, stream>>>(ptrs, cvt, xx, z);
-  k_conv<<<LL, DI, 0, stream>>>(xx, c[2], c[3], xc);
-  k_proj<<<KD*(LL/PT), 256, 0, stream>>>(xc, c[4], dts, Bb, Cb);
-  if (chBits == 8){
-    k_scanA<8><<<KD*256, 192, 0, stream>>>(xc, dts, Bb, c[7], c[5], c[6], cumD, Harr);
-    k_scan2<8><<<NC/256, 256, 0, stream>>>(c[7], cumD, Harr);
-    k_scanB<8><<<KD*256, 192, 0, stream>>>(xc, dts, Bb, Cb, c[7], c[5], c[6], Harr, ydir);
-  } else {
-    k_scanA<6><<<KD*64, 192, 0, stream>>>(xc, dts, Bb, c[7], c[5], c[6], cumD, Harr);
-    k_scan2<6><<<NC/256, 256, 0, stream>>>(c[7], cumD, Harr);
-    k_scanB<6><<<KD*64, 192, 0, stream>>>(xc, dts, Bb, Cb, c[7], c[5], c[6], Harr, ydir);
-  }
-  k_out<<<LL/OT, 192, 0, stream>>>(ydir, xc, z, c[8], c[9], c[10], c[11], d_out,
-                                   (const unsigned short*)d_in[0]);
+  float* Harr = cumD + (size_t)CHN*NCH;
+  float* ydir = Harr + (size_t)CHN*NC;
+  int*   bar  = (int*)(ydir + (size_t)KD*LL*DI);
+
+  MArgs a;
+  for (int i = 0; i < 12; i++) a.p[i] = d_in[i];
+  a.cvt = cvt; a.xx = xx; a.z = z; a.xc = xc;
+  a.dts = dts; a.Bb = Bb; a.Cb = Cb;
+  a.cumD = cumD; a.Harr = Harr; a.ydir = ydir;
+  a.bar = bar; a.out = d_out;
+
+  hipMemsetAsync(bar, 0, 256, stream);
+  hipLaunchKernelGGL(k_mega, dim3(GRID), dim3(BLK), 0, stream, a);
 }
```

After: 525.5 us. +138.7%, slower.
